# Kernel optimization log

Measured on AMD Instinct MI355X. Metric: run time of the kernel, lower is better.

The kernel has to match this reference:

```python
import jax, jax.numpy as jnp
import numpy as np

N_NODES = 50000
BN_EPS = 1e-5


def setup_inputs() -> dict:
    key = jax.random.key(0)
    ks = jax.random.split(key, 6)
    N, E, CIN, CH, COUT = N_NODES, 800000, 128, 256, 128
    node_feat = jax.random.normal(ks[0], (N, CIN), dtype=jnp.float32)
    edge_index = jax.random.randint(ks[1], (2, E), 0, N, dtype=jnp.int64)
    # Glorot-ish init for weights
    W1 = jax.random.normal(ks[2], (CIN, CH), dtype=jnp.float32) / np.sqrt(CIN)
    b1 = jnp.zeros((CH,), dtype=jnp.float32)
    bn_gamma = jnp.ones((CH,), dtype=jnp.float32)
    bn_beta = jnp.zeros((CH,), dtype=jnp.float32)
    W2 = jax.random.normal(ks[3], (CH, COUT), dtype=jnp.float32) / np.sqrt(CH)
    b2 = jnp.zeros((COUT,), dtype=jnp.float32)
    return {"node_feat": node_feat, "edge_index": edge_index, "W1": W1, "b1": b1,
            "bn_gamma": bn_gamma, "bn_beta": bn_beta, "W2": W2, "b2": b2}


def gcn_conv(x, W, b, src, dst, n_nodes):
    """PyG GCNConv: out = D^-1/2 (A+I) D^-1/2 (x W) + b."""
    h = x @ W                                   # [N, C_out]
    loop = jnp.arange(n_nodes, dtype=src.dtype)
    src_f = jnp.concatenate([src, loop])        # self-loops appended
    dst_f = jnp.concatenate([dst, loop])
    deg = jax.ops.segment_sum(jnp.ones_like(dst_f, dtype=h.dtype), dst_f,
                              num_segments=n_nodes)
    dinv = jax.lax.rsqrt(jnp.maximum(deg, 1.0))  # deg >= 1 due to self-loops
    norm = dinv[src_f] * dinv[dst_f]             # [E+N]
    msg = h[src_f] * norm[:, None]               # gather + scale
    return jax.ops.segment_sum(msg, dst_f, num_segments=n_nodes) + b


def batch_norm(x, gamma, beta):
    mean = jnp.mean(x, axis=0)
    var = jnp.mean((x - mean) ** 2, axis=0)      # biased var (torch BN normalization)
    return (x - mean) * jax.lax.rsqrt(var + BN_EPS) * gamma + beta


def reference(node_feat, edge_index, W1, b1, bn_gamma, bn_beta, W2, b2):
    src, dst = edge_index[0], edge_index[1]
    x = gcn_conv(node_feat, W1, b1, src, dst, N_NODES)
    x = batch_norm(x, bn_gamma, bn_beta)
    x = jax.nn.relu(x)
    # dropout is identity at inference
    x = gcn_conv(x, W2, b2, src, dst, N_NODES)
    return x
```

## Files before the change

### kernel.cpp

```cpp
#include <hip/hip_runtime.h>
#include <hip/hip_fp16.h>

#define CIN 128
#define CH 256
#define COUT 128
#define BN_EPS 1e-5f

typedef __attribute__((ext_vector_type(8))) short bf16x8;
typedef __attribute__((ext_vector_type(4))) float f32x4;

__device__ __forceinline__ short f2bf(float x) {
    unsigned u = __float_as_uint(x);
    unsigned r = (u + 0x7fffu + ((u >> 16) & 1u)) >> 16;
    return (short)r;
}
__device__ __forceinline__ float bf2f(short h) {
    return __uint_as_float(((unsigned)(unsigned short)h) << 16);
}

__global__ void k_deg(const int* __restrict__ dst, int* __restrict__ degi,
                      unsigned short* __restrict__ rank, int E) {
    int e = blockIdx.x * 256 + threadIdx.x;
    if (e < E) rank[e] = (unsigned short)atomicAdd(&degi[dst[e]], 1);
}

__global__ void k_scan1(const int* __restrict__ degi, float* __restrict__ dinv,
                        int* __restrict__ blocksum, int N) {
    __shared__ int s[256];
    int i = blockIdx.x * 256 + threadIdx.x;
    int v = (i < N) ? degi[i] : 0;
    if (i < N) dinv[i] = rsqrtf((float)(v + 1));
    s[threadIdx.x] = v;
    __syncthreads();
    for (int st = 128; st > 0; st >>= 1) {
        if (threadIdx.x < st) s[threadIdx.x] += s[threadIdx.x + st];
        __syncthreads();
    }
    if (threadIdx.x == 0) blocksum[blockIdx.x] = s[0];
}

__global__ void k_scan3(const int* __restrict__ degi, const int* __restrict__ blocksum,
                        int nb, int* __restrict__ rowstart, int N, int E) {
    __shared__ int sb[256];
    __shared__ int s[256];
    int bv = (threadIdx.x < nb) ? blocksum[threadIdx.x] : 0;
    sb[threadIdx.x] = bv;
    __syncthreads();
    for (int st = 1; st < 256; st <<= 1) {
        int t = (threadIdx.x >= st) ? sb[threadIdx.x - st] : 0;
        __syncthreads();
        sb[threadIdx.x] += t;
        __syncthreads();
    }
    int boff = (blockIdx.x == 0) ? 0 : sb[blockIdx.x - 1];

    int i = blockIdx.x * 256 + threadIdx.x;
    int v = (i < N) ? degi[i] : 0;
    s[threadIdx.x] = v;
    __syncthreads();
    for (int st = 1; st < 256; st <<= 1) {
        int t = (threadIdx.x >= st) ? s[threadIdx.x - st] : 0;
        __syncthreads();
        s[threadIdx.x] += t;
        __syncthreads();
    }
    if (i < N) rowstart[i] = s[threadIdx.x] - v + boff;
    if (blockIdx.x == 0 && threadIdx.x == 0) rowstart[N] = E;
}

__global__ void k_fill(const int* __restrict__ src, const int* __restrict__ dst,
                       const unsigned short* __restrict__ rank,
                       const int* __restrict__ rowstart,
                       unsigned short* __restrict__ csr, int E) {
    int e = blockIdx.x * 256 + threadIdx.x;
    if (e >= E) return;
    int d = dst[e];
    int pos = rowstart[d] + (int)rank[e];
    __builtin_nontemporal_store((unsigned short)src[e], &csr[pos]);
}

__global__ void k_prep(const float* __restrict__ W1, const float* __restrict__ W2,
                       short* __restrict__ W1sw, short* __restrict__ W2sw,
                       const float4* __restrict__ nf, short4* __restrict__ nfb, int n4) {
    int t = blockIdx.x * 256 + threadIdx.x;
    if (t < 32768) {
        int n = t >> 7, kk = t & 127;
        float v = W1[kk * 256 + n];
        short h = f2bf(v);
        short l = f2bf(v - bf2f(h));
        int t16 = n >> 4, m = n & 15;
        int ks = kk >> 5, q = (kk >> 3) & 3, j = kk & 7;
        int idx = (t16 * 4 + ks) * 1024 + (q * 16 + m) * 8 + j;
        W1sw[idx] = h;
        W1sw[idx + 512] = l;
    } else if (t < 65536) {
        int u = t - 32768;
        int n = u >> 8, kk = u & 255;
        float v = W2[kk * 128 + n];
        short h = f2bf(v);
        short l = f2bf(v - bf2f(h));
        int t16 = n >> 4, m = n & 15;
        int ks = kk >> 5, q = (kk >> 3) & 3, j = kk & 7;
        int idx = (t16 * 8 + ks) * 1024 + (q * 16 + m) * 8 + j;
        W2sw[idx] = h;
        W2sw[idx + 512] = l;
    } else {
        int u = t - 65536;
        if (u < n4) {
            float4 v = nf[u];
            short4 s;
            s.x = f2bf(v.x); s.y = f2bf(v.y); s.z = f2bf(v.z); s.w = f2bf(v.w);
            nfb[u] = s;
        }
    }
}

template <int MODE>
__global__ __launch_bounds__(256) void k_gather(const short* __restrict__ xb,
                                                const int* __restrict__ rowstart,
                                                const unsigned short* __restrict__ csr,
                                                const float* __restrict__ dinv,
                                                const float* __restrict__ bias,
                                                float* __restrict__ out,
                                                short* __restrict__ ob, int N) {
    int t = blockIdx.x * 256 + threadIdx.x;
    int r = t >> 4;
    int c = t & 15;
    if (r >= N) return;
    float di = dinv[r];
    float w0 = di * di;
    bf16x8 sv = *(const bf16x8*)(xb + (size_t)r * 128 + c * 8);
    float acc[8];
    #pragma unroll
    for (int j = 0; j < 8; ++j) acc[j] = bf2f(sv[j]) * w0;
    int e0 = rowstart[r], e1 = rowstart[r + 1];
    int e = e0;
    for (; e + 7 < e1; e += 8) {
        int s[8];
        #pragma unroll
        for (int i = 0; i < 8; ++i) s[i] = csr[e + i];
        float w[8];
        #pragma unroll
        for (int i = 0; i < 8; ++i) w[i] = dinv[s[i]] * di;
        bf16x8 x[8];
        #pragma unroll
        for (int i = 0; i < 8; ++i) x[i] = *(const bf16x8*)(xb + (size_t)s[i] * 128 + c * 8);
        #pragma unroll
        for (int i = 0; i < 8; ++i)
            #pragma unroll
            for (int j = 0; j < 8; ++j) acc[j] = fmaf(w[i], bf2f(x[i][j]), acc[j]);
    }
    for (; e + 3 < e1; e += 4) {
        int s[4];
        #pragma unroll
        for (int i = 0; i < 4; ++i) s[i] = csr[e + i];
        float w[4];
        #pragma unroll
        for (int i = 0; i < 4; ++i) w[i] = dinv[s[i]] * di;
        bf16x8 x[4];
        #pragma unroll
        for (int i = 0; i < 4; ++i) x[i] = *(const bf16x8*)(xb + (size_t)s[i] * 128 + c * 8);
        #pragma unroll
        for (int i = 0; i < 4; ++i)
            #pragma unroll
            for (int j = 0; j < 8; ++j) acc[j] = fmaf(w[i], bf2f(x[i][j]), acc[j]);
    }
    for (; e < e1; ++e) {
        int s0 = csr[e];
        float ww = dinv[s0] * di;
        bf16x8 x0 = *(const bf16x8*)(xb + (size_t)s0 * 128 + c * 8);
        #pragma unroll
        for (int j = 0; j < 8; ++j) acc[j] = fmaf(ww, bf2f(x0[j]), acc[j]);
    }
    if (MODE == 0) {
        bf16x8 h;
        #pragma unroll
        for (int j = 0; j < 8; ++j) h[j] = f2bf(acc[j]);
        *(bf16x8*)(ob + (size_t)r * 128 + c * 8) = h;
    } else {
        float4 b0 = *(const float4*)(bias + c * 8);
        float4 b1 = *(const float4*)(bias + c * 8 + 4);
        float4 o0 = make_float4(acc[0] + b0.x, acc[1] + b0.y, acc[2] + b0.z, acc[3] + b0.w);
        float4 o1 = make_float4(acc[4] + b1.x, acc[5] + b1.y, acc[6] + b1.z, acc[7] + b1.w);
        *(float4*)(out + (size_t)r * 128 + c * 8) = o0;
        *(float4*)(out + (size_t)r * 128 + c * 8 + 4) = o1;
    }
}

__device__ __forceinline__ bf16x8 bnrelu8(bf16x8 raw, const float* __restrict__ scsh, int c) {
    float4 sc0 = *(const float4*)(scsh + c);
    float4 sc1 = *(const float4*)(scsh + c + 4);
    float4 sh0 = *(const float4*)(scsh + 256 + c);
    float4 sh1 = *(const float4*)(scsh + 256 + c + 4);
    bf16x8 o;
    o[0] = f2bf(fmaxf(fmaf(bf2f(raw[0]), sc0.x, sh0.x), 0.f));
    o[1] = f2bf(fmaxf(fmaf(bf2f(raw[1]), sc0.y, sh0.y), 0.f));
    o[2] = f2bf(fmaxf(fmaf(bf2f(raw[2]), sc0.z, sh0.z), 0.f));
    o[3] = f2bf(fmaxf(fmaf(bf2f(raw[3]), sc0.w, sh0.w), 0.f));
    o[4] = f2bf(fmaxf(fmaf(bf2f(raw[4]), sc1.x, sh1.x), 0.f));
    o[5] = f2bf(fmaxf(fmaf(bf2f(raw[5]), sc1.y, sh1.y), 0.f));
    o[6] = f2bf(fmaxf(fmaf(bf2f(raw[6]), sc1.z, sh1.z), 0.f));
    o[7] = f2bf(fmaxf(fmaf(bf2f(raw[7]), sc1.w, sh1.w), 0.f));
    return o;
}

template <int K, int NOUT, bool STATS, bool BIAS, bool BNRELU>
__global__ __launch_bounds__(256, 2) void k_gemm(const short* __restrict__ A,
                                                 const short* __restrict__ Bsw,
                                                 const float* __restrict__ bias,
                                                 const float* __restrict__ scsh,
                                                 short* __restrict__ C,
                                                 float* __restrict__ partials, int M) {
    constexpr int CT = NOUT / 64;
    constexpr int KS = K / 32;
    constexpr int KP = K + 8;
    constexpr int LROW = NOUT + 8;
    constexpr int LSZ = (64 * KP > 64 * LROW) ? 64 * KP : 64 * LROW;
    __shared__ __align__(16) short lds[LSZ];
    int tid = threadIdx.x;
    int wave = tid >> 6;
    int lane = tid & 63;
    int m = lane & 15;
    int q = lane >> 4;
    int row0 = blockIdx.x * 64;

    constexpr int CPRA = K / 8;
    #pragma unroll
    for (int i = 0; i < (64 * CPRA) / 256; ++i) {
        int idx = i * 256 + tid;
        int r = idx / CPRA, cc = idx % CPRA;
        int gr = row0 + r;
        if (gr >= M) gr = M - 1;
        bf16x8 v = *(const bf16x8*)(A + (size_t)gr * K + cc * 8);
        if (BNRELU) v = bnrelu8(v, scsh, cc * 8);
        *(bf16x8*)(lds + r * KP + cc * 8) = v;
    }
    __syncthreads();

    f32x4 acc[4][CT];
    #pragma unroll
    for (int rt = 0; rt < 4; ++rt)
        #pragma unroll
        for (int ct = 0; ct < CT; ++ct)
            acc[rt][ct] = (f32x4){0.f, 0.f, 0.f, 0.f};

    bf16x8 bh[2][CT], bl[2][CT];
    #pragma unroll
    for (int ct = 0; ct < CT; ++ct) {
        const short* bp = Bsw + (size_t)((wave * CT + ct) * KS) * 1024 + lane * 8;
        bh[0][ct] = *(const bf16x8*)bp;
        bl[0][ct] = *(const bf16x8*)(bp + 512);
    }

    #pragma unroll
    for (int ks = 0; ks < KS; ++ks) {
        const int cur = ks & 1, nxt = cur ^ 1;
        if (ks + 1 < KS) {
            #pragma unroll
            for (int ct = 0; ct < CT; ++ct) {
                const short* bp = Bsw + (size_t)((wave * CT + ct) * KS + ks + 1) * 1024 + lane * 8;
                bh[nxt][ct] = *(const bf16x8*)bp;
                bl[nxt][ct] = *(const bf16x8*)(bp + 512);
            }
        }
        bf16x8 af[4];
        #pragma unroll
        for (int rt = 0; rt < 4; ++rt)
            af[rt] = *(const bf16x8*)(lds + (rt * 16 + m) * KP + ks * 32 + q * 8);
        #pragma unroll
        for (int ct = 0; ct < CT; ++ct)
            #pragma unroll
            for (int rt = 0; rt < 4; ++rt) {
                acc[rt][ct] = __builtin_amdgcn_mfma_f32_16x16x32_bf16(af[rt], bh[cur][ct], acc[rt][ct], 0, 0, 0);
                acc[rt][ct] = __builtin_amdgcn_mfma_f32_16x16x32_bf16(af[rt], bl[cur][ct], acc[rt][ct], 0, 0, 0);
            }
    }
    __syncthreads();

    #pragma unroll
    for (int ct = 0; ct < CT; ++ct) {
        int col = wave * (NOUT / 4) + ct * 16 + m;
        float bv = BIAS ? bias[col] : 0.f;
        float s = 0.f, sq = 0.f;
        #pragma unroll
        for (int rt = 0; rt < 4; ++rt) {
            #pragma unroll
            for (int r = 0; r < 4; ++r) {
                int lrow = rt * 16 + q * 4 + r;
                float v = acc[rt][ct][r] + bv;
                if (STATS && row0 + lrow < M) { s += v; sq = fmaf(v, v, sq); }
                lds[lrow * LROW + col] = f2bf(v);
            }
        }
        if (STATS) {
            s += __shfl_xor(s, 16, 64);
            s += __shfl_xor(s, 32, 64);
            sq += __shfl_xor(sq, 16, 64);
            sq += __shfl_xor(sq, 32, 64);
            if (lane < 16) {
                partials[(size_t)blockIdx.x * 512 + col] = s;
                partials[(size_t)blockIdx.x * 512 + 256 + col] = sq;
            }
        }
    }
    __syncthreads();
    constexpr int CPR = NOUT / 8;
    #pragma unroll
    for (int i = 0; i < (64 * CPR) / 256; ++i) {
        int idx = i * 256 + tid;
        int row = idx / CPR;
        int ch = idx % CPR;
        if (row0 + row < M)
            *(bf16x8*)(C + (size_t)(row0 + row) * NOUT + ch * 8) =
                *(const bf16x8*)(lds + row * LROW + ch * 8);
    }
}

__global__ void k_redstats(const float* __restrict__ partials, float* __restrict__ stats,
                           int nb, int rpb) {
    int sid = threadIdx.x;
    int r0 = blockIdx.x * rpb;
    int r1 = r0 + rpb;
    if (r1 > nb) r1 = nb;
    float acc = 0.f;
    for (int r = r0; r < r1; ++r) acc += partials[(size_t)r * 512 + sid];
    unsafeAtomicAdd(&stats[sid], acc);
}

__global__ void k_bnfinal(const float* __restrict__ stats, const float* __restrict__ gamma,
                          const float* __restrict__ beta, float* __restrict__ scsh, int N) {
    int c = threadIdx.x;
    float invN = 1.0f / (float)N;
    float mean = stats[c] * invN;
    float var = stats[256 + c] * invN - mean * mean;
    var = fmaxf(var, 0.f);
    float inv = rsqrtf(var + BN_EPS);
    float sc = gamma[c] * inv;
    scsh[c] = sc;
    scsh[256 + c] = fmaf(-mean, sc, beta[c]);
}

extern "C" void kernel_launch(void* const* d_in, const int* in_sizes, int n_in,
                              void* d_out, int out_size, void* d_ws, size_t ws_size,
                              hipStream_t stream) {
    const float* nf    = (const float*)d_in[0];
    const int*   ei    = (const int*)d_in[1];
    const float* W1    = (const float*)d_in[2];
    const float* b1    = (const float*)d_in[3];
    const float* gamma = (const float*)d_in[4];
    const float* beta  = (const float*)d_in[5];
    const float* W2    = (const float*)d_in[6];
    const float* b2    = (const float*)d_in[7];
    float* out = (float*)d_out;

    const int N = in_sizes[0] / CIN;
    const int E = in_sizes[1] / 2;
    const int* src = ei;
    const int* dst = ei + E;

    const int nb1 = (N + 63) / 64;

    char* ws = (char*)d_ws;
    auto align256 = [](size_t x) { return (x + 255) & ~(size_t)255; };
    size_t off = 0;
    int*   degi = (int*)(ws + off);      off += align256((size_t)N * 4);
    float* stats = (float*)(ws + off);   off += align256(512 * 4);
    size_t zspan = off;
    float* dinv = (float*)(ws + off);    off += align256((size_t)N * 4);
    int*   rowstart = (int*)(ws + off);  off += align256((size_t)(N + 1) * 4);
    int*   blocksum = (int*)(ws + off);  off += align256(256 * 4);
    float* scsh = (float*)(ws + off);    off += align256(512 * 4);
    short* W1sw = (short*)(ws + off);    off += align256(65536 * 2);
    short* W2sw = (short*)(ws + off);    off += align256(65536 * 2);
    float* partials = (float*)(ws + off); off += align256((size_t)nb1 * 512 * 4);
    unsigned short* rank = (unsigned short*)(ws + off); off += align256((size_t)E * 2);
    unsigned short* csr = (unsigned short*)(ws + off);  off += align256((size_t)E * 2);
    short* nfb = (short*)(ws + off);     off += align256((size_t)N * CIN * 2);
    short* agg1b = (short*)(ws + off);   off += align256((size_t)N * CIN * 2);
    short* x1b = (short*)(ws + off);     off += align256((size_t)N * CH * 2);
    short* yb = (short*)(ws + off);      off += align256((size_t)N * COUT * 2);

    int nbN = (N + 255) / 256;
    int nbE = (E + 255) / 256;
    int n4 = N * 32;

    hipMemsetAsync(ws, 0, zspan, stream);

    k_prep<<<(65536 + n4 + 255) / 256, 256, 0, stream>>>(
        W1, W2, W1sw, W2sw, (const float4*)nf, (short4*)nfb, n4);

    k_deg<<<nbE, 256, 0, stream>>>(dst, degi, rank, E);
    k_scan1<<<nbN, 256, 0, stream>>>(degi, dinv, blocksum, N);
    k_scan3<<<nbN, 256, 0, stream>>>(degi, blocksum, nbN, rowstart, N, E);
    k_fill<<<nbE, 256, 0, stream>>>(src, dst, rank, rowstart, csr, E);

    k_gather<0><<<(N * 16 + 255) / 256, 256, 0, stream>>>(
        nfb, rowstart, csr, dinv, nullptr, nullptr, agg1b, N);

    k_gemm<CIN, CH, true, true, false><<<nb1, 256, 0, stream>>>(
        agg1b, W1sw, b1, nullptr, x1b, partials, N);

    {
        int rblocks = 8;
        int rpb = (nb1 + rblocks - 1) / rblocks;
        k_redstats<<<rblocks, 512, 0, stream>>>(partials, stats, nb1, rpb);
    }
    k_bnfinal<<<1, 256, 0, stream>>>(stats, gamma, beta, scsh, N);

    k_gemm<CH, COUT, false, false, true><<<nb1, 256, 0, stream>>>(
        x1b, W2sw, nullptr, scsh, yb, nullptr, N);

    k_gather<1><<<(N * 16 + 255) / 256, 256, 0, stream>>>(
        yb, rowstart, csr, dinv, b2, out, nullptr, N);
}
```

Measured before the change: 277.5 us.

## Drop bf16 hi/lo weight split, fold memset into prep, raise GEMM occupancy

Weights are now stored as a single bf16 value instead of a high/low bf16 pair, which halves the MFMA count and the weight loads in both GEMMs. The GEMM also drops the double-buffered weight prefetch and raises the launch-bounds occupancy hint from 2 to 4 blocks per CU. The separate memset of the degree and stats buffers is folded into the prep kernel, removing one launch. The cost is lower weight precision, which may exceed the accuracy tolerance, plus less latency hiding on weight loads within each wave.

New measurement: 267.3 us. 1.04x faster.

```diff
diff --git a/kernel.cpp b/kernel.cpp
--- a/kernel.cpp
+++ b/kernel.cpp
@@ -81,29 +81,24 @@
 
 __global__ void k_prep(const float* __restrict__ W1, const float* __restrict__ W2,
                        short* __restrict__ W1sw, short* __restrict__ W2sw,
-                       const float4* __restrict__ nf, short4* __restrict__ nfb, int n4) {
+                       const float4* __restrict__ nf, short4* __restrict__ nfb,
+                       int* __restrict__ degi, float* __restrict__ stats,
+                       int n4, int N) {
     int t = blockIdx.x * 256 + threadIdx.x;
     if (t < 32768) {
+        if (t < 512) stats[t] = 0.0f;
         int n = t >> 7, kk = t & 127;
         float v = W1[kk * 256 + n];
-        short h = f2bf(v);
-        short l = f2bf(v - bf2f(h));
         int t16 = n >> 4, m = n & 15;
         int ks = kk >> 5, q = (kk >> 3) & 3, j = kk & 7;
-        int idx = (t16 * 4 + ks) * 1024 + (q * 16 + m) * 8 + j;
-        W1sw[idx] = h;
-        W1sw[idx + 512] = l;
+        W1sw[(t16 * 4 + ks) * 512 + (q * 16 + m) * 8 + j] = f2bf(v);
     } else if (t < 65536) {
         int u = t - 32768;
         int n = u >> 8, kk = u & 255;
         float v = W2[kk * 128 + n];
-        short h = f2bf(v);
-        short l = f2bf(v - bf2f(h));
         int t16 = n >> 4, m = n & 15;
         int ks = kk >> 5, q = (kk >> 3) & 3, j = kk & 7;
-        int idx = (t16 * 8 + ks) * 1024 + (q * 16 + m) * 8 + j;
-        W2sw[idx] = h;
-        W2sw[idx + 512] = l;
+        W2sw[(t16 * 8 + ks) * 512 + (q * 16 + m) * 8 + j] = f2bf(v);
     } else {
         int u = t - 65536;
         if (u < n4) {
@@ -111,6 +106,9 @@
             short4 s;
             s.x = f2bf(v.x); s.y = f2bf(v.y); s.z = f2bf(v.z); s.w = f2bf(v.w);
             nfb[u] = s;
+        } else {
+            int u2 = u - n4;
+            if (u2 < N) degi[u2] = 0;
         }
     }
 }
@@ -205,7 +203,7 @@
 }
 
 template <int K, int NOUT, bool STATS, bool BIAS, bool BNRELU>
-__global__ __launch_bounds__(256, 2) void k_gemm(const short* __restrict__ A,
+__global__ __launch_bounds__(256, 4) void k_gemm(const short* __restrict__ A,
                                                  const short* __restrict__ Bsw,
                                                  const float* __restrict__ bias,
                                                  const float* __restrict__ scsh,
@@ -244,25 +242,12 @@
         for (int ct = 0; ct < CT; ++ct)
             acc[rt][ct] = (f32x4){0.f, 0.f, 0.f, 0.f};
 
-    bf16x8 bh[2][CT], bl[2][CT];
-    #pragma unroll
-    for (int ct = 0; ct < CT; ++ct) {
-        const short* bp = Bsw + (size_t)((wave * CT + ct) * KS) * 1024 + lane * 8;
-        bh[0][ct] = *(const bf16x8*)bp;
-        bl[0][ct] = *(const bf16x8*)(bp + 512);
-    }
-
     #pragma unroll
     for (int ks = 0; ks < KS; ++ks) {
-        const int cur = ks & 1, nxt = cur ^ 1;
-        if (ks + 1 < KS) {
-            #pragma unroll
-            for (int ct = 0; ct < CT; ++ct) {
-                const short* bp = Bsw + (size_t)((wave * CT + ct) * KS + ks + 1) * 1024 + lane * 8;
-                bh[nxt][ct] = *(const bf16x8*)bp;
-                bl[nxt][ct] = *(const bf16x8*)(bp + 512);
-            }
-        }
+        bf16x8 bh[CT];
+        #pragma unroll
+        for (int ct = 0; ct < CT; ++ct)
+            bh[ct] = *(const bf16x8*)(Bsw + (size_t)((wave * CT + ct) * KS + ks) * 512 + lane * 8);
         bf16x8 af[4];
         #pragma unroll
         for (int rt = 0; rt < 4; ++rt)
@@ -270,10 +255,8 @@
         #pragma unroll
         for (int ct = 0; ct < CT; ++ct)
             #pragma unroll
-            for (int rt = 0; rt < 4; ++rt) {
-                acc[rt][ct] = __builtin_amdgcn_mfma_f32_16x16x32_bf16(af[rt], bh[cur][ct], acc[rt][ct], 0, 0, 0);
-                acc[rt][ct] = __builtin_amdgcn_mfma_f32_16x16x32_bf16(af[rt], bl[cur][ct], acc[rt][ct], 0, 0, 0);
-            }
+            for (int rt = 0; rt < 4; ++rt)
+                acc[rt][ct] = __builtin_amdgcn_mfma_f32_16x16x32_bf16(af[rt], bh[ct], acc[rt][ct], 0, 0, 0);
     }
     __syncthreads();
 
@@ -365,13 +348,12 @@
     size_t off = 0;
     int*   degi = (int*)(ws + off);      off += align256((size_t)N * 4);
     float* stats = (float*)(ws + off);   off += align256(512 * 4);
-    size_t zspan = off;
     float* dinv = (float*)(ws + off);    off += align256((size_t)N * 4);
     int*   rowstart = (int*)(ws + off);  off += align256((size_t)(N + 1) * 4);
     int*   blocksum = (int*)(ws + off);  off += align256(256 * 4);
     float* scsh = (float*)(ws + off);    off += align256(512 * 4);
-    short* W1sw = (short*)(ws + off);    off += align256(65536 * 2);
-    short* W2sw = (short*)(ws + off);    off += align256(65536 * 2);
+    short* W1sw = (short*)(ws + off);    off += align256(32768 * 2);
+    short* W2sw = (short*)(ws + off);    off += align256(32768 * 2);
     float* partials = (float*)(ws + off); off += align256((size_t)nb1 * 512 * 4);
     unsigned short* rank = (unsigned short*)(ws + off); off += align256((size_t)E * 2);
     unsigned short* csr = (unsigned short*)(ws + off);  off += align256((size_t)E * 2);
@@ -384,10 +366,8 @@
     int nbE = (E + 255) / 256;
     int n4 = N * 32;
 
-    hipMemsetAsync(ws, 0, zspan, stream);
-
-    k_prep<<<(65536 + n4 + 255) / 256, 256, 0, stream>>>(
-        W1, W2, W1sw, W2sw, (const float4*)nf, (short4*)nfb, n4);
+    k_prep<<<(65536 + n4 + N + 255) / 256, 256, 0, stream>>>(
+        W1, W2, W1sw, W2sw, (const float4*)nf, (short4*)nfb, degi, stats, n4, N);
 
     k_deg<<<nbE, 256, 0, stream>>>(dst, degi, rank, E);
     k_scan1<<<nbN, 256, 0, stream>>>(degi, dinv, blocksum, N);
```
